# Kernel tuning notes

Hardware: AMD Instinct MI355X
Metric: run time of the kernel (lower is better)

The kernel has to match this reference:

```python
import jax, jax.numpy as jnp
import numpy as np
import math

D_MODEL, N_HEADS, D_HEAD, D_MLP = 768, 12, 64, 3072
LN_EPS = 1e-5
INIT_STD = 0.02


def gelu_new(x):
    # GPT-2 'new' gelu: 0.5*x*(1+tanh(sqrt(2/pi)*(x+0.044715*x^3)))
    c = math.sqrt(2.0 / math.pi)
    return 0.5 * x * (1.0 + jnp.tanh(c * (x + 0.044715 * jnp.power(x, 3.0))))


def layer_norm(x, w, b):
    mu = jnp.mean(x, axis=-1, keepdims=True)
    xc = x - mu
    scale = jnp.sqrt(jnp.mean(xc * xc, axis=-1, keepdims=True) + LN_EPS)
    return (xc / scale) * w + b


def setup_inputs() -> dict:
    key = jax.random.key(0)
    ks = jax.random.split(key, 8)
    resid_pre = jax.random.normal(ks[0], (8, 1024, D_MODEL), dtype=jnp.float32)
    W_Q = jax.random.normal(ks[1], (N_HEADS, D_MODEL, D_HEAD), dtype=jnp.float32) * INIT_STD
    W_K = jax.random.normal(ks[2], (N_HEADS, D_MODEL, D_HEAD), dtype=jnp.float32) * INIT_STD
    W_V = jax.random.normal(ks[3], (N_HEADS, D_MODEL, D_HEAD), dtype=jnp.float32) * INIT_STD
    W_O = jax.random.normal(ks[4], (N_HEADS, D_HEAD, D_MODEL), dtype=jnp.float32) * INIT_STD
    W_in = jax.random.normal(ks[5], (D_MODEL, D_MLP), dtype=jnp.float32) * INIT_STD
    W_out = jax.random.normal(ks[6], (D_MLP, D_MODEL), dtype=jnp.float32) * INIT_STD
    return {
        'resid_pre': resid_pre,
        'ln1_w': jnp.ones((D_MODEL,), jnp.float32), 'ln1_b': jnp.zeros((D_MODEL,), jnp.float32),
        'W_Q': W_Q, 'b_Q': jnp.zeros((N_HEADS, D_HEAD), jnp.float32),
        'W_K': W_K, 'b_K': jnp.zeros((N_HEADS, D_HEAD), jnp.float32),
        'W_V': W_V, 'b_V': jnp.zeros((N_HEADS, D_HEAD), jnp.float32),
        'W_O': W_O, 'b_O': jnp.zeros((D_MODEL,), jnp.float32),
        'ln2_w': jnp.ones((D_MODEL,), jnp.float32), 'ln2_b': jnp.zeros((D_MODEL,), jnp.float32),
        'W_in': W_in, 'b_in': jnp.zeros((D_MLP,), jnp.float32),
        'W_out': W_out, 'b_out': jnp.zeros((D_MODEL,), jnp.float32),
    }


def attention(x, W_Q, b_Q, W_K, b_K, W_V, b_V, W_O, b_O):
    # x: [b, s, d_model]
    q = jnp.einsum('bsd,hde->bshe', x, W_Q) + b_Q
    k = jnp.einsum('bsd,hde->bshe', x, W_K) + b_K
    v = jnp.einsum('bsd,hde->bshe', x, W_V) + b_V
    scores = jnp.einsum('bqhe,bkhe->bhqk', q, k) / math.sqrt(D_HEAD)
    s = x.shape[1]
    causal = jnp.triu(jnp.ones((s, s), dtype=bool), k=1)
    scores = jnp.where(causal, -jnp.inf, scores)
    pattern = jax.nn.softmax(scores, axis=-1)
    pattern = jnp.where(jnp.isnan(pattern), 0.0, pattern)
    z = jnp.einsum('bhqk,bkhe->bqhe', pattern, v)
    # per-head projection then sum over heads; b_O/n_heads per head sums to b_O
    return jnp.einsum('bqhe,hed->bqd', z, W_O) + b_O


def reference(resid_pre, ln1_w, ln1_b, W_Q, b_Q, W_K, b_K, W_V, b_V, W_O, b_O,
              ln2_w, ln2_b, W_in, b_in, W_out, b_out):
    normed1 = layer_norm(resid_pre, ln1_w, ln1_b)
    attn_out = attention(normed1, W_Q, b_Q, W_K, b_K, W_V, b_V, W_O, b_O)
    residual = resid_pre + attn_out
    normed2 = layer_norm(residual, ln2_w, ln2_b)
    pre = jnp.einsum('bsd,dm->bsm', normed2, W_in) + b_in
    mlp_out = jnp.einsum('bsm,md->bsd', gelu_new(pre), W_out) + b_out
    return residual + mlp_out
```

## Files before the change

### kernel.cpp

```cpp
#include <hip/hip_runtime.h>
#include <hip/hip_bf16.h>
#include <stdint.h>
#include <math.h>

typedef __bf16 bf16x8 __attribute__((ext_vector_type(8)));
typedef float f32x4 __attribute__((ext_vector_type(4)));
using bf16 = __hip_bfloat16;

__device__ inline float bf2f(bf16 x) { return __bfloat162float(x); }
__device__ inline bf16 f2bf(float x) { return __float2bfloat16(x); }

__device__ inline f32x4 mfma16(bf16x8 a, bf16x8 b, f32x4 c) {
  return __builtin_amdgcn_mfma_f32_16x16x32_bf16(a, b, c, 0, 0, 0);
}

__device__ inline void async16(const bf16* g, bf16* l) {
  __builtin_amdgcn_global_load_lds(
      (const __attribute__((address_space(1))) unsigned int*)g,
      (__attribute__((address_space(3))) unsigned int*)l, 16, 0, 0);
}

__device__ inline float gelu_new(float x) {
  float u2 = 1.5957691216057308f * (x + 0.044715f * x * x * x);
  float e = __expf(u2);
  float t = 1.0f - 2.0f * __builtin_amdgcn_rcpf(e + 1.0f);
  return 0.5f * x * (1.0f + t);
}

__device__ inline void ln_body(const float* __restrict__ x, const float* __restrict__ w,
                               const float* __restrict__ bb, bf16* __restrict__ out,
                               int row, int t, float* red) {
  size_t base = (size_t)row * 768;
  float v0 = x[base + t];
  float v1 = x[base + t + 256];
  float v2 = x[base + t + 512];
  float s = v0 + v1 + v2;
  float ss = v0 * v0 + v1 * v1 + v2 * v2;
#pragma unroll
  for (int off = 32; off > 0; off >>= 1) {
    s += __shfl_down(s, off, 64);
    ss += __shfl_down(ss, off, 64);
  }
  int wv = t >> 6, ln = t & 63;
  if (ln == 0) { red[wv] = s; red[4 + wv] = ss; }
  __syncthreads();
  s = red[0] + red[1] + red[2] + red[3];
  ss = red[4] + red[5] + red[6] + red[7];
  float mu = s * (1.0f / 768.0f);
  float var = ss * (1.0f / 768.0f) - mu * mu;
  float rinv = rsqrtf(var + 1e-5f);
  out[base + t]       = f2bf((v0 - mu) * rinv * w[t]       + bb[t]);
  out[base + t + 256] = f2bf((v1 - mu) * rinv * w[t + 256] + bb[t + 256]);
  out[base + t + 512] = f2bf((v2 - mu) * rinv * w[t + 512] + bb[t + 512]);
}

__global__ __launch_bounds__(256) void ln_kernel(const float* __restrict__ x,
                                                 const float* __restrict__ w,
                                                 const float* __restrict__ bb,
                                                 bf16* __restrict__ out) {
  __shared__ float red[8];
  ln_body(x, w, bb, out, blockIdx.x, threadIdx.x, red);
}

__device__ inline void transpose_body(const float* __restrict__ in, bf16* __restrict__ out,
                                      int R, int C, int bx, int by, int t,
                                      float (*tile)[33]) {
  int tx = t & 31, ty = t >> 5;
  int r0 = bx * 32, c0 = by * 32;
#pragma unroll
  for (int j = 0; j < 32; j += 8)
    tile[ty + j][tx] = in[(size_t)(r0 + ty + j) * C + c0 + tx];
  __syncthreads();
#pragma unroll
  for (int j = 0; j < 32; j += 8)
    out[(size_t)(c0 + ty + j) * R + r0 + tx] = f2bf(tile[tx][ty + j]);
}

__global__ __launch_bounds__(256) void prep_all(
    const float* __restrict__ resid_pre, const float* __restrict__ ln1_w,
    const float* __restrict__ ln1_b, bf16* __restrict__ n1,
    const float* __restrict__ Wq, const float* __restrict__ Wk,
    const float* __restrict__ Wv, bf16* __restrict__ Wqkv_t,
    const float* __restrict__ W_O, bf16* __restrict__ Wo_t,
    const float* __restrict__ W_in, bf16* __restrict__ Win_t,
    const float* __restrict__ W_out, bf16* __restrict__ Wout_t,
    const float* __restrict__ bq, const float* __restrict__ bk,
    const float* __restrict__ bv, float* __restrict__ bias_qkv) {
  __shared__ float tile[32][33];
  const int t = threadIdx.x;
  int bid = blockIdx.x;
  if (bid < 8192) {
    ln_body(resid_pre, ln1_w, ln1_b, n1, bid, t, &tile[0][0]);
    return;
  }
  bid -= 8192;
  if (bid < 1728) {
    int z = bid / 48, r = bid - z * 48;
    int which = z / 12, h = z - which * 12;
    const float* W = (which == 0) ? Wq : ((which == 1) ? Wk : Wv);
    transpose_body(W + (size_t)h * 768 * 64,
                   Wqkv_t + (size_t)which * 589824 + (size_t)h * 64 * 768,
                   768, 64, r % 24, r / 24, t, tile);
    return;
  }
  bid -= 1728;
  if (bid < 576) {
    transpose_body(W_O, Wo_t, 768, 768, bid % 24, bid / 24, t, tile);
    return;
  }
  bid -= 576;
  if (bid < 2304) {
    transpose_body(W_in, Win_t, 768, 3072, bid % 24, bid / 24, t, tile);
    return;
  }
  bid -= 2304;
  if (bid < 2304) {
    transpose_body(W_out, Wout_t, 3072, 768, bid % 96, bid / 96, t, tile);
    return;
  }
  bid -= 2304;
  int i = bid * 256 + t;
  if (i < 2304)
    bias_qkv[i] = (i < 768) ? bq[i] : ((i < 1536) ? bk[i - 768] : bv[i - 1536]);
}

enum { MODE_QKV = 0, MODE_ADDF = 2, MODE_GELU = 3 };

template <int MODE, int MROWS>
__global__ __launch_bounds__(256) void gemm_bt(
    const bf16* __restrict__ A, const bf16* __restrict__ BT,
    const float* __restrict__ bias,
    const float* __restrict__ addend,
    float* __restrict__ out_f32,
    bf16* __restrict__ out_bf16,
    int M, int N, int K) {
  constexpr int MI = MROWS / 32;
  __shared__ __align__(16) bf16 smem[(MROWS + 128) * 64];
  bf16* Alds = smem;
  bf16* Blds = smem + MROWS * 64;
  const int t = threadIdx.x;
  const int wave = t >> 6, lane = t & 63;
  const int lm = lane & 15, quad = lane >> 4;
  const int wm = wave >> 1, wn = wave & 1;
  const int m0 = blockIdx.x * MROWS, n0 = blockIdx.y * 128;

  f32x4 acc[MI][4] = {};

  for (int k0 = 0; k0 < K; k0 += 64) {
#pragma unroll
    for (int i = 0; i < MI; i++) {
      int c = i * 256 + t;
      int r = c >> 3, cs = c & 7;
      async16(A + (size_t)(m0 + r) * K + k0 + ((cs ^ (r & 7)) << 3), &Alds[c * 8]);
    }
#pragma unroll
    for (int i = 0; i < 4; i++) {
      int c = i * 256 + t;
      int r = c >> 3, cs = c & 7;
      async16(BT + (size_t)(n0 + r) * K + k0 + ((cs ^ (r & 7)) << 3), &Blds[c * 8]);
    }
    __syncthreads();
#pragma unroll
    for (int kk = 0; kk < 64; kk += 32) {
      const int cbase = kk >> 3;
      bf16x8 af[MI], bfr[4];
#pragma unroll
      for (int mi = 0; mi < MI; mi++)
        af[mi] = *(const bf16x8*)&Alds[(wm * (MROWS / 2) + mi * 16 + lm) * 64 +
                                       (((cbase + quad) ^ (lm & 7)) << 3)];
#pragma unroll
      for (int ni = 0; ni < 4; ni++)
        bfr[ni] = *(const bf16x8*)&Blds[(wn * 64 + ni * 16 + lm) * 64 +
                                        (((cbase + quad) ^ (lm & 7)) << 3)];
#pragma unroll
      for (int mi = 0; mi < MI; mi++)
#pragma unroll
        for (int ni = 0; ni < 4; ni++)
          acc[mi][ni] = mfma16(af[mi], bfr[ni], acc[mi][ni]);
    }
    __syncthreads();
  }

  float bv[4];
#pragma unroll
  for (int ni = 0; ni < 4; ni++) bv[ni] = bias[n0 + wn * 64 + ni * 16 + lm];

  float* sc = (float*)smem + wave * 1088;
  const bool vseg = (MODE == MODE_QKV) && ((n0 + wn * 64) >= 1536);

#pragma unroll
  for (int mi = 0; mi < MI; mi++) {
    __syncthreads();
#pragma unroll
    for (int ni = 0; ni < 4; ni++)
#pragma unroll
      for (int reg = 0; reg < 4; reg++) {
        float val = acc[mi][ni][reg] + bv[ni];
        if (vseg) sc[(ni * 16 + lm) * 17 + quad * 4 + reg] = val;
        else      sc[(quad * 4 + reg) * 67 + ni * 16 + lm] = val;
      }
    __syncthreads();

    if (!vseg) {
#pragma unroll
      for (int p = 0; p < 2; p++) {
        int rl = p * 8 + (lane >> 3);
        int cl = (lane & 7) * 8;
        float v[8];
#pragma unroll
        for (int j = 0; j < 8; j++) v[j] = sc[rl * 67 + cl + j];
        int rm = m0 + wm * (MROWS / 2) + mi * 16 + rl;
        int cn0 = n0 + wn * 64 + cl;
        if constexpr (MODE == MODE_GELU) {
          bf16x8 o;
#pragma unroll
          for (int j = 0; j < 8; j++) o[j] = (__bf16)gelu_new(v[j]);
          *(bf16x8*)(out_bf16 + (size_t)rm * N + cn0) = o;
        } else if constexpr (MODE == MODE_ADDF) {
          size_t idx = (size_t)rm * N + cn0;
          f32x4 a0 = *(const f32x4*)(addend + idx);
          f32x4 a1 = *(const f32x4*)(addend + idx + 4);
          f32x4 o0, o1;
#pragma unroll
          for (int j = 0; j < 4; j++) { o0[j] = v[j] + a0[j]; o1[j] = v[4 + j] + a1[j]; }
          *(f32x4*)(out_f32 + idx) = o0;
          *(f32x4*)(out_f32 + idx + 4) = o1;
        } else {
          int seg = cn0 / 768;
          int lnn = cn0 - seg * 768;
          int h2 = lnn >> 6, e0 = lnn & 63;
          int b2 = rm >> 10, sq = rm & 1023;
          float scale = (seg == 0) ? 0.125f : 1.0f;
          bf16x8 o;
#pragma unroll
          for (int j = 0; j < 8; j++) o[j] = (__bf16)(v[j] * scale);
          *(bf16x8*)(out_bf16 + (size_t)seg * 6291456 +
                     (((size_t)(b2 * 12 + h2) * 1024 + sq) << 6) + e0) = o;
        }
      }
    } else {
#pragma unroll
      for (int p = 0; p < 2; p++) {
        float v[8];
#pragma unroll
        for (int j = 0; j < 8; j++) v[j] = sc[lane * 17 + p * 8 + j];
        int e_he = n0 + wn * 64 + lane;
        int lnn = e_he - 1536;
        int h2 = lnn >> 6, e2 = lnn & 63;
        int s0 = m0 + wm * (MROWS / 2) + mi * 16 + p * 8;
        int b2 = s0 >> 10, sq = s0 & 1023;
        bf16x8 o;
#pragma unroll
        for (int j = 0; j < 8; j++) o[j] = (__bf16)v[j];
        *(bf16x8*)(out_bf16 + (size_t)2 * 6291456 +
                   (((size_t)(b2 * 12 + h2) * 64 + e2) << 10) + sq) = o;
      }
    }
  }
}

#define READ_A(H, BUF) do {                                                           \
  _Pragma("unroll")                                                                   \
  for (int f_ = 0; f_ < 4; f_++) {                                                    \
    _Pragma("unroll")                                                                 \
    for (int k_ = 0; k_ < 2; k_++)                                                    \
      Af[H][f_][k_] = *(const bf16x8*)&sm[(BUF) * 32768 + (H) * 8192 +                \
                                          (aRow + f_ * 16) * 64 +                     \
                                          (((k_ * 4 + quad) ^ lms) << 3)];            \
  }                                                                                   \
} while (0)

#define READ_B(H, BUF) do {                                                           \
  _Pragma("unroll")                                                                   \
  for (int g_ = 0; g_ < 2; g_++) {                                                    \
    _Pragma("unroll")                                                                 \
    for (int k_ = 0; k_ < 2; k_++)                                                    \
      Bf[H][g_][k_] = *(const bf16x8*)&sm[(BUF) * 32768 + 16384 + (H) * 8192 +        \
                                          (bRow + g_ * 16) * 64 +                     \
                                          (((k_ * 4 + quad) ^ lms) << 3)];            \
  }                                                                                   \
} while (0)

#define DO_MFMA(AH, BH) do {                                                          \
  __builtin_amdgcn_s_setprio(1);                                                      \
  _Pragma("unroll")                                                                   \
  for (int k_ = 0; k_ < 2; k_++) {                                                    \
    _Pragma("unroll")                                                                 \
    for (int f_ = 0; f_ < 4; f_++) {                                                  \
      _Pragma("unroll")                                                               \
      for (int g_ = 0; g_ < 2; g_++)                                                  \
        acc[AH][f_][BH][g_] =                                                         \
            mfma16(Af[AH][f_][k_], Bf[BH][g_][k_], acc[AH][f_][BH][g_]);              \
    }                                                                                 \
  }                                                                                   \
  __builtin_amdgcn_s_setprio(0);                                                      \
} while (0)

template <int MODE>
__global__ __launch_bounds__(512, 2) void gemm256(
    const bf16* __restrict__ A, const bf16* __restrict__ BT,
    const float* __restrict__ bias, bf16* __restrict__ out, int N) {
  __shared__ __align__(16) bf16 sm[65536];
  const int tid = threadIdx.x;
  const int wave = tid >> 6, lane = tid & 63;
  const int lm = lane & 15, quad = lane >> 4, lms = lm & 7;
  const int wm = wave >> 2, wn = wave & 3;

  const int cpx = gridDim.x >> 3;
  const int swz = (blockIdx.x & 7) * cpx + (blockIdx.x >> 3);
  const int m0 = (swz & 31) * 256;
  const int n0 = (swz >> 5) * 256;

  const int aRow = wm * 64 + lm;
  const int bRow = wn * 32 + lm;

  const int r0 = tid >> 3;
  const int of0 = (((tid & 7) ^ (r0 & 7)) << 3);
  const bf16* sA = A + (size_t)(m0 + r0) * 768 + of0;
  const bf16* sB = BT + (size_t)(n0 + r0) * 768 + of0;

  auto STA = [&](int bb, int ah, int t2) {
    bf16* d = sm + bb * 32768 + ah * 8192 + tid * 8;
    const bf16* s = sA + ah * 98304 + t2 * 64;
    async16(s, d);
    async16(s + 49152, d + 4096);
  };
  auto STB = [&](int bb, int bh, int t2) {
    bf16* d = sm + bb * 32768 + 16384 + bh * 8192 + tid * 8;
    const bf16* s = sB + bh * 98304 + t2 * 64;
    async16(s, d);
    async16(s + 49152, d + 4096);
  };

  f32x4 acc[2][4][2][2] = {};
  bf16x8 Af[2][4][2];
  bf16x8 Bf[2][2][2];

  STA(0, 0, 0); STB(0, 0, 0); STA(0, 1, 0); STB(0, 1, 0);
  STA(1, 0, 1); STB(1, 0, 1);
  asm volatile("s_waitcnt vmcnt(4)" ::: "memory");
  __builtin_amdgcn_s_barrier();
  READ_A(0, 0);
  READ_B(0, 0);

#pragma unroll 2
  for (int tt = 0; tt < 12; ++tt) {
    const int c = tt & 1, nb = c ^ 1;
    READ_B(1, c);
    if (tt + 1 < 12) STA(nb, 1, tt + 1);
    __builtin_amdgcn_s_barrier();
    DO_MFMA(0, 0);
    __builtin_amdgcn_s_barrier();
    READ_A(1, c);
    if (tt + 1 < 12) STB(nb, 1, tt + 1);
    __builtin_amdgcn_s_barrier();
    DO_MFMA(0, 1);
    if (tt + 1 < 12) asm volatile("s_waitcnt vmcnt(4)" ::: "memory");
    __builtin_amdgcn_s_barrier();
    if (tt + 1 < 12) READ_A(0, nb);
    if (tt + 2 < 12) STA(c, 0, tt + 2);
    __builtin_amdgcn_s_barrier();
    DO_MFMA(1, 0);
    __builtin_amdgcn_s_barrier();
    if (tt + 1 < 12) READ_B(0, nb);
    if (tt + 2 < 12) STB(c, 0, tt + 2);
    __builtin_amdgcn_s_barrier();
    DO_MFMA(1, 1);
    if (tt + 1 < 12) {
      if (tt + 2 < 12) asm volatile("s_waitcnt vmcnt(4)" ::: "memory");
      else             asm volatile("s_waitcnt vmcnt(0)" ::: "memory");
    }
    __builtin_amdgcn_s_barrier();
  }

  float bvv[2][2];
#pragma unroll
  for (int bh2 = 0; bh2 < 2; bh2++)
#pragma unroll
    for (int g = 0; g < 2; g++)
      bvv[bh2][g] = bias[n0 + bh2 * 128 + wn * 32 + g * 16 + lm];

  float* sc = (float*)sm + wave * 1088;

  if constexpr (MODE == MODE_GELU) {
#pragma unroll
    for (int mi = 0; mi < 8; mi++) {
      const int ah = mi >> 2, f = mi & 3;
#pragma unroll
      for (int bh2 = 0; bh2 < 2; bh2++)
#pragma unroll
        for (int g = 0; g < 2; g++)
#pragma unroll
          for (int reg = 0; reg < 4; reg++)
            sc[(quad * 4 + reg) * 68 + bh2 * 32 + g * 16 + lm] =
                acc[ah][f][bh2][g][reg] + bvv[bh2][g];
#pragma unroll
      for (int p = 0; p < 2; p++) {
        int slot = p * 64 + lane;
        int rw = slot >> 3, c8 = (slot & 7) * 8;
        f32x4 u0 = *(const f32x4*)&sc[rw * 68 + c8];
        f32x4 u1 = *(const f32x4*)&sc[rw * 68 + c8 + 4];
        int grow = m0 + ah * 128 + wm * 64 + f * 16 + rw;
        int bh3 = c8 >> 5, cc = c8 & 31;
        int gcol = n0 + bh3 * 128 + wn * 32 + cc;
        bf16x8 o;
#pragma unroll
        for (int j = 0; j < 4; j++) { o[j] = (__bf16)gelu_new(u0[j]); o[4 + j] = (__bf16)gelu_new(u1[j]); }
        *(bf16x8*)(out + (size_t)grow * N + gcol) = o;
      }
    }
  } else {
    const int seg = n0 / 768;
    const float scale = (seg == 0) ? 0.125f : 1.0f;
    if (seg < 2) {
      bf16* qout = out + (size_t)seg * 6291456;
#pragma unroll
      for (int mi = 0; mi < 8; mi++) {
        const int ah = mi >> 2, f = mi & 3;
#pragma unroll
        for (int bh2 = 0; bh2 < 2; bh2++)
#pragma unroll
          for (int g = 0; g < 2; g++)
#pragma unroll
            for (int reg = 0; reg < 4; reg++)
              sc[(quad * 4 + reg) * 68 + bh2 * 32 + g * 16 + lm] =
                  (acc[ah][f][bh2][g][reg] + bvv[bh2][g]) * scale;
#pragma unroll
        for (int p = 0; p < 2; p++) {
          int slot = p * 64 + lane;
          int rw = slot >> 3, c8 = (slot & 7) * 8;
          f32x4 u0 = *(const f32x4*)&sc[rw * 68 + c8];
          f32x4 u1 = *(const f32x4*)&sc[rw * 68 + c8 + 4];
          int grow = m0 + ah * 128 + wm * 64 + f * 16 + rw;
          int bh3 = c8 >> 5, cc = c8 & 31;
          int gcol = n0 + bh3 * 128 + wn * 32 + cc;
          int lnn = gcol - seg * 768;
          int h2 = lnn >> 6, e0 = lnn & 63;
          int b2 = grow >> 10, sq = grow & 1023;
          bf16x8 o;
#pragma unroll
          for (int j = 0; j < 4; j++) { o[j] = (__bf16)u0[j]; o[4 + j] = (__bf16)u1[j]; }
          *(bf16x8*)(qout + (((size_t)(b2 * 12 + h2) * 1024 + sq) << 6) + e0) = o;
        }
      }
    } else {
#pragma unroll
      for (int mi = 0; mi < 8; mi++) {
        const int ah = mi >> 2, f = mi & 3;
#pragma unroll
        for (int bh2 = 0; bh2 < 2; bh2++)
#pragma unroll
          for (int g = 0; g < 2; g++)
#pragma unroll
            for (int reg = 0; reg < 4; reg++)
              sc[(bh2 * 32 + g * 16 + lm) * 17 + quad * 4 + reg] =
                  acc[ah][f][bh2][g][reg] + bvv[bh2][g];
#pragma unroll
        for (int p = 0; p < 2; p++) {
          float v[8];
#pragma unroll
          for (int j = 0; j < 8; j++) v[j] = sc[lane * 17 + p * 8 + j];
          int bh3 = lane >> 5, cc = lane & 31;
          int gcol = n0 + bh3 * 128 + wn * 32 + cc;
          int lnn = gcol - 1536;
          int h2 = lnn >> 6, e2 = lnn & 63;
          int s0 = m0 + ah * 128 + wm * 64 + f * 16 + p * 8;
          int b2 = s0 >> 10, sq = s0 & 1023;
          bf16x8 o;
#pragma unroll
          for (int j = 0; j < 8; j++) o[j] = (__bf16)v[j];
          *(bf16x8*)(out + (size_t)2 * 6291456 +
                     (((size_t)(b2 * 12 + h2) * 64 + e2) << 10) + sq) = o;
        }
      }
    }
  }
}

__global__ __launch_bounds__(256) void attn_kernel(const bf16* __restrict__ q,
                                                   const bf16* __restrict__ k,
                                                   const bf16* __restrict__ vt,
                                                   bf16* __restrict__ z) {
  const int S = 1024, E = 64;
  __shared__ __align__(16) bf16 Klds[64 * 64];
  __shared__ __align__(16) bf16 Vlds[64 * 64];
  __shared__ __align__(16) bf16 Plds[4 * 16 * 64];
  const int pb = blockIdx.x;
  const int bh = blockIdx.y;
  const int t = threadIdx.x;
  const int wave = t >> 6, lane = t & 63;
  const int lm = lane & 15, quad = lane >> 4;
  const size_t bh_se = (size_t)bh * S * E;
  const int b = bh / 12, h = bh - b * 12;

  for (int seg = 0; seg < 2; seg++) {
    const int qt = seg ? (15 - pb) : pb;
    const int qrow = qt * 64 + wave * 16 + lm;
    bf16x8 qf0 = *(const bf16x8*)(q + bh_se + (size_t)qrow * E + quad * 8);
    bf16x8 qf1 = *(const bf16x8*)(q + bh_se + (size_t)qrow * E + 32 + quad * 8);

    f32x4 acco[4] = {};
    float lsum[4] = {0.f, 0.f, 0.f, 0.f};

    for (int kt = 0; kt <= qt; kt++) {
#pragma unroll
      for (int i = 0; i < 2; i++) {
        int c = i * 256 + t;
        int r = c >> 3, cs = c & 7;
        int sw = (cs ^ (r & 7)) << 3;
        async16(k + bh_se + (size_t)(kt * 64 + r) * E + sw, &Klds[c * 8]);
        async16(vt + bh_se + (size_t)r * S + kt * 64 + sw, &Vlds[c * 8]);
      }
      __syncthreads();

      f32x4 accs[4] = {};
#pragma unroll
      for (int ni = 0; ni < 4; ni++) {
        int row = ni * 16 + lm;
        bf16x8 kf0 = *(const bf16x8*)&Klds[row * 64 + ((quad ^ (lm & 7)) << 3)];
        bf16x8 kf1 = *(const bf16x8*)&Klds[row * 64 + (((4 + quad) ^ (lm & 7)) << 3)];
        accs[ni] = mfma16(qf0, kf0, accs[ni]);
        accs[ni] = mfma16(qf1, kf1, accs[ni]);
      }

      float pv[4][4];
      const int qg = wave * 16 + quad * 4;
      if (kt == qt) {
#pragma unroll
        for (int ni = 0; ni < 4; ni++)
#pragma unroll
          for (int reg = 0; reg < 4; reg++) {
            float e_ = __expf(accs[ni][reg]);
            pv[ni][reg] = ((ni * 16 + lm) > (qg + reg)) ? 0.f : e_;
          }
      } else {
#pragma unroll
        for (int ni = 0; ni < 4; ni++)
#pragma unroll
          for (int reg = 0; reg < 4; reg++)
            pv[ni][reg] = __expf(accs[ni][reg]);
      }

#pragma unroll
      for (int ni = 0; ni < 4; ni++)
#pragma unroll
        for (int reg = 0; reg < 4; reg++) {
          lsum[reg] += pv[ni][reg];
          int pr = quad * 4 + reg;
          int ce = ni * 16 + lm;
          Plds[wave * 1024 + pr * 64 + (((ce >> 3) ^ (pr & 7)) << 3) + (ce & 7)] =
              f2bf(pv[ni][reg]);
        }
      __syncthreads();

      bf16x8 pf0 = *(const bf16x8*)&Plds[wave * 1024 + lm * 64 + ((quad ^ (lm & 7)) << 3)];
      bf16x8 pf1 = *(const bf16x8*)&Plds[wave * 1024 + lm * 64 + (((4 + quad) ^ (lm & 7)) << 3)];
#pragma unroll
      for (int ni = 0; ni < 4; ni++) {
        int row = ni * 16 + lm;
        bf16x8 vf0 = *(const bf16x8*)&Vlds[row * 64 + ((quad ^ (lm & 7)) << 3)];
        bf16x8 vf1 = *(const bf16x8*)&Vlds[row * 64 + (((4 + quad) ^ (lm & 7)) << 3)];
        acco[ni] = mfma16(pf0, vf0, acco[ni]);
        acco[ni] = mfma16(pf1, vf1, acco[ni]);
      }
      __syncthreads();
    }

#pragma unroll
    for (int reg = 0; reg < 4; reg++) {
#pragma unroll
      for (int off = 1; off < 16; off <<= 1) lsum[reg] += __shfl_xor(lsum[reg], off, 16);
    }
    float rl[4];
#pragma unroll
    for (int reg = 0; reg < 4; reg++) rl[reg] = 1.0f / lsum[reg];

#pragma unroll
    for (int ni = 0; ni < 4; ni++)
#pragma unroll
      for (int reg = 0; reg < 4; reg++) {
        int srow = qt * 64 + wave * 16 + quad * 4 + reg;
        size_t idx = (((size_t)(b * 1024 + srow) * 12 + h) << 6) + ni * 16 + lm;
        z[idx] = f2bf(acco[ni][reg] * rl[reg]);
      }
  }
}

extern "C" void kernel_launch(void* const* d_in, const int* in_sizes, int n_in,
                              void* d_out, int out_size, void* d_ws, size_t ws_size,
                              hipStream_t stream) {
  (void)in_sizes; (void)n_in; (void)out_size; (void)ws_size;
  const float* resid_pre = (const float*)d_in[0];
  const float* ln1_w = (const float*)d_in[1];
  const float* ln1_b = (const float*)d_in[2];
  const float* W_Q = (const float*)d_in[3];
  const float* b_Q = (const float*)d_in[4];
  const float* W_K = (const float*)d_in[5];
  const float* b_K = (const float*)d_in[6];
  const float* W_V = (const float*)d_in[7];
  const float* b_V = (const float*)d_in[8];
  const float* W_O = (const float*)d_in[9];
  const float* b_O = (const float*)d_in[10];
  const float* ln2_w = (const float*)d_in[11];
  const float* ln2_b = (const float*)d_in[12];
  const float* W_in = (const float*)d_in[13];
  const float* b_in = (const float*)d_in[14];
  const float* W_out = (const float*)d_in[15];
  const float* b_out = (const float*)d_in[16];

  char* ws = (char*)d_ws;
  const size_t EB = (size_t)8192 * 768;
  bf16* n1     = (bf16*)(ws);
  bf16* qb     = (bf16*)(ws + EB * 2);
  bf16* zb     = (bf16*)(ws + EB * 8);
  float* resid = (float*)(ws + EB * 10);
  bf16* act    = (bf16*)(ws + EB * 2);
  char* wsw = ws + EB * 14;
  bf16* Wqkv_t = (bf16*)(wsw);
  bf16* Wo_t   = (bf16*)(wsw + 3 * 1179648);
  bf16* Win_t  = (bf16*)(wsw + 4 * 1179648);
  bf16* Wout_t = (bf16*)(wsw + 4 * 1179648 + 4718592);
  float* bias_qkv = (float*)(wsw + 4 * 1179648 + 4718592 + 9437184);
  bf16* kb  = qb + EB;
  bf16* vtb = qb + 2 * EB;

  prep_all<<<15113, 256, 0, stream>>>(resid_pre, ln1_w, ln1_b, n1,
                                      W_Q, W_K, W_V, Wqkv_t,
                                      W_O, Wo_t, W_in, Win_t, W_out, Wout_t,
                                      b_Q, b_K, b_V, bias_qkv);

  gemm256<MODE_QKV><<<288, 512, 0, stream>>>(n1, Wqkv_t, bias_qkv, qb, 2304);

  attn_kernel<<<dim3(8, 96), 256, 0, stream>>>(qb, kb, vtb, zb);

  gemm_bt<MODE_ADDF, 64><<<dim3(128, 6), 256, 0, stream>>>(
      zb, Wo_t, b_O, resid_pre, resid, nullptr, 8192, 768, 768);

  ln_kernel<<<8192, 256, 0, stream>>>(resid, ln2_w, ln2_b, n1);

  gemm256<MODE_GELU><<<384, 512, 0, stream>>>(n1, Win_t, b_in, act, 3072);

  gemm_bt<MODE_ADDF, 64><<<dim3(128, 6), 256, 0, stream>>>(
      act, Wout_t, b_out, resid, (float*)d_out, nullptr, 8192, 768, 3072);
}
```

Measured before the change: 386.0 us.

## Restructure GEMM mainloop to single A fragment buffer, cutting register pressure

The GEMM main loop now keeps one A fragment set instead of two and splits the B fragments into two named buffers. Each A half is reloaded from LDS just before its MFMA phases, and the B0 half is read twice per iteration. The vmcnt and lgkmcnt wait points are reworked to match the new load schedule. This frees VGPRs to sustain 2 blocks of 512 threads per CU, at the cost of extra LDS reads and less prefetch overlap across iterations.

```diff
diff --git a/kernel.cpp b/kernel.cpp
--- a/kernel.cpp
+++ b/kernel.cpp
@@ -259,29 +259,29 @@
   }
 }
 
-#define READ_A(H, BUF) do {                                                           \
+#define READ_A(BUF, H) do {                                                           \
   _Pragma("unroll")                                                                   \
   for (int f_ = 0; f_ < 4; f_++) {                                                    \
     _Pragma("unroll")                                                                 \
     for (int k_ = 0; k_ < 2; k_++)                                                    \
-      Af[H][f_][k_] = *(const bf16x8*)&sm[(BUF) * 32768 + (H) * 8192 +                \
-                                          (aRow + f_ * 16) * 64 +                     \
-                                          (((k_ * 4 + quad) ^ lms) << 3)];            \
+      Af[f_][k_] = *(const bf16x8*)&sm[(BUF) * 32768 + (H) * 8192 +                   \
+                                       (aRow + f_ * 16) * 64 +                        \
+                                       (((k_ * 4 + quad) ^ lms) << 3)];               \
   }                                                                                   \
 } while (0)
 
-#define READ_B(H, BUF) do {                                                           \
+#define READ_Bx(BUF, H, DST) do {                                                     \
   _Pragma("unroll")                                                                   \
   for (int g_ = 0; g_ < 2; g_++) {                                                    \
     _Pragma("unroll")                                                                 \
     for (int k_ = 0; k_ < 2; k_++)                                                    \
-      Bf[H][g_][k_] = *(const bf16x8*)&sm[(BUF) * 32768 + 16384 + (H) * 8192 +        \
-                                          (bRow + g_ * 16) * 64 +                     \
-                                          (((k_ * 4 + quad) ^ lms) << 3)];            \
+      DST[g_][k_] = *(const bf16x8*)&sm[(BUF) * 32768 + 16384 + (H) * 8192 +          \
+                                        (bRow + g_ * 16) * 64 +                       \
+                                        (((k_ * 4 + quad) ^ lms) << 3)];              \
   }                                                                                   \
 } while (0)
 
-#define DO_MFMA(AH, BH) do {                                                          \
+#define DO_MFMA(AH, BH, BFR) do {                                                     \
   __builtin_amdgcn_s_setprio(1);                                                      \
   _Pragma("unroll")                                                                   \
   for (int k_ = 0; k_ < 2; k_++) {                                                    \
@@ -290,7 +290,7 @@
       _Pragma("unroll")                                                               \
       for (int g_ = 0; g_ < 2; g_++)                                                  \
         acc[AH][f_][BH][g_] =                                                         \
-            mfma16(Af[AH][f_][k_], Bf[BH][g_][k_], acc[AH][f_][BH][g_]);              \
+            mfma16(Af[f_][k_], BFR[g_][k_], acc[AH][f_][BH][g_]);                     \
     }                                                                                 \
   }                                                                                   \
   __builtin_amdgcn_s_setprio(0);                                                      \
@@ -333,43 +333,45 @@
   };
 
   f32x4 acc[2][4][2][2] = {};
-  bf16x8 Af[2][4][2];
-  bf16x8 Bf[2][2][2];
+  bf16x8 Af[4][2];
+  bf16x8 Bf0[2][2];
+  bf16x8 Bf1[2][2];
 
   STA(0, 0, 0); STB(0, 0, 0); STA(0, 1, 0); STB(0, 1, 0);
   STA(1, 0, 1); STB(1, 0, 1);
-  asm volatile("s_waitcnt vmcnt(4)" ::: "memory");
+  asm volatile("s_waitcnt vmcnt(8)" ::: "memory");
   __builtin_amdgcn_s_barrier();
-  READ_A(0, 0);
-  READ_B(0, 0);
 
 #pragma unroll 2
   for (int tt = 0; tt < 12; ++tt) {
     const int c = tt & 1, nb = c ^ 1;
-    READ_B(1, c);
+    READ_A(c, 0);
+    READ_Bx(c, 0, Bf0);
     if (tt + 1 < 12) STA(nb, 1, tt + 1);
     __builtin_amdgcn_s_barrier();
-    DO_MFMA(0, 0);
-    __builtin_amdgcn_s_barrier();
-    READ_A(1, c);
+    DO_MFMA(0, 0, Bf0);
+    asm volatile("s_waitcnt lgkmcnt(0)" ::: "memory");
+    if (tt + 1 < 12) asm volatile("s_waitcnt vmcnt(6)" ::: "memory");
+    else             asm volatile("s_waitcnt vmcnt(0)" ::: "memory");
+    __builtin_amdgcn_s_barrier();
+    READ_Bx(c, 1, Bf1);
     if (tt + 1 < 12) STB(nb, 1, tt + 1);
     __builtin_amdgcn_s_barrier();
-    DO_MFMA(0, 1);
-    if (tt + 1 < 12) asm volatile("s_waitcnt vmcnt(4)" ::: "memory");
-    __builtin_amdgcn_s_barrier();
-    if (tt + 1 < 12) READ_A(0, nb);
+    DO_MFMA(0, 1, Bf1);
+    asm volatile("s_waitcnt lgkmcnt(0)" ::: "memory");
+    __builtin_amdgcn_s_barrier();
+    READ_A(c, 1);
+    READ_Bx(c, 0, Bf0);
     if (tt + 2 < 12) STA(c, 0, tt + 2);
     __builtin_amdgcn_s_barrier();
-    DO_MFMA(1, 0);
-    __builtin_amdgcn_s_barrier();
-    if (tt + 1 < 12) READ_B(0, nb);
+    DO_MFMA(1, 0, Bf0);
+    asm volatile("s_waitcnt lgkmcnt(0)" ::: "memory");
+    __builtin_amdgcn_s_barrier();
     if (tt + 2 < 12) STB(c, 0, tt + 2);
     __builtin_amdgcn_s_barrier();
-    DO_MFMA(1, 1);
-    if (tt + 1 < 12) {
-      if (tt + 2 < 12) asm volatile("s_waitcnt vmcnt(4)" ::: "memory");
-      else             asm volatile("s_waitcnt vmcnt(0)" ::: "memory");
-    }
+    DO_MFMA(1, 1, Bf1);
+    if (tt + 2 < 12)      asm volatile("s_waitcnt vmcnt(8)" ::: "memory");
+    else if (tt + 1 < 12) asm volatile("s_waitcnt vmcnt(4)" ::: "memory");
     __builtin_amdgcn_s_barrier();
   }
 
```

Result: faster. 353.0 us (-8.5%).
